# Kernel tuning notes

Hardware: AMD Instinct MI355X
Metric: run time of the kernel (lower is better)

The kernel has to match this reference:

```python
import jax, jax.numpy as jnp
import numpy as np

B, E, N, M = 2, 512, 4096, 4096

def setup_inputs() -> dict:
    key = jax.random.key(0)
    ks = jax.random.split(key, 8)
    s = 1.0 / np.sqrt(E)
    return {
        "src_embedding": jax.random.normal(ks[0], (B, E, N), jnp.float32),
        "tgt_embedding": jax.random.normal(ks[1], (B, E, M), jnp.float32),
        "src": jax.random.normal(ks[2], (B, 3, N), jnp.float32),
        "tgt": jax.random.normal(ks[3], (B, 3, M), jnp.float32),
        "Wq": jax.random.normal(ks[4], (E, E), jnp.float32) * s,
        "bq": jax.random.normal(ks[5], (E,), jnp.float32) * s,
        "Wk": jax.random.normal(ks[6], (E, E), jnp.float32) * s,
        "bk": jax.random.normal(ks[7], (E,), jnp.float32) * s,
    }

def reference(src_embedding, tgt_embedding, src, tgt, Wq, bq, Wk, bk):
    # query/key: [B, N, E] after transpose + Linear (y = x @ W^T + b)
    q = jnp.einsum('ben,fe->bnf', src_embedding, Wq) + bq
    k = jnp.einsum('bem,fe->bmf', tgt_embedding, Wk) + bk
    # pairwise_distance[b,n,m] = -||q_n||^2 + 2 q_n.k_m - ||k_m||^2 = -||q_n - k_m||^2
    inner = jnp.einsum('bne,bme->bnm', q, k)          # [B, N, M]
    qq = jnp.sum(q * q, axis=-1)                      # [B, N]
    kk = jnp.sum(k * k, axis=-1)                      # [B, M]
    pairwise = 2.0 * inner - qq[:, :, None] - kk[:, None, :]
    scores = jax.nn.softmax(pairwise, axis=2)         # softmax over keys (M)
    # src_corr = tgt @ scores^T : [B, 3, N]
    src_corr = jnp.einsum('bdm,bnm->bdn', tgt, scores)
    return (src, src_corr)
```

## Files before the change

### kernel.cpp

```cpp
#include <hip/hip_runtime.h>


typedef _Float16 f16;
typedef __attribute__((ext_vector_type(8))) _Float16 f16x8;
typedef __attribute__((ext_vector_type(4))) float f32x4;

constexpr int B_ = 2, E_ = 512, N_ = 4096, M_ = 4096;
constexpr int MCH = 8;
constexpr float WSCALE = 64.0f;

__device__ __forceinline__ f32x4 mfma16(f16x8 a, f16x8 b, f32x4 c) {
  return __builtin_amdgcn_mfma_f32_16x16x32_f16(a, b, c, 0, 0, 0);
}
__device__ __forceinline__ void gll16(const void* g, void* l) {
  __builtin_amdgcn_global_load_lds(
      (const __attribute__((address_space(1))) unsigned int*)g,
      (__attribute__((address_space(3))) unsigned int*)l, 16, 0, 0);
}
__device__ __forceinline__ void waitv8() { asm volatile("s_waitcnt vmcnt(8)" ::: "memory"); }
__device__ __forceinline__ void waitv0() { asm volatile("s_waitcnt vmcnt(0)" ::: "memory"); }
__device__ __forceinline__ f32x4 vmax4(f32x4 a, f32x4 b) {
  f32x4 r;
  r[0] = fmaxf(a[0], b[0]); r[1] = fmaxf(a[1], b[1]);
  r[2] = fmaxf(a[2], b[2]); r[3] = fmaxf(a[3], b[3]);
  return r;
}
__device__ __forceinline__ f32x4 vexp4(f32x4 a) {
  f32x4 r;
  r[0] = __expf(a[0]); r[1] = __expf(a[1]);
  r[2] = __expf(a[2]); r[3] = __expf(a[3]);
  return r;
}


__global__ void k_split_w(const float* __restrict__ Wq, const float* __restrict__ Wk,
                          f16* __restrict__ WqH, f16* __restrict__ WqL,
                          f16* __restrict__ WkH, f16* __restrict__ WkL) {
  int i = blockIdx.x * 256 + threadIdx.x;
  float a = Wq[i] * WSCALE;
  f16 ah = (f16)a; WqH[i] = ah; WqL[i] = (f16)(a - (float)ah);
  float b = Wk[i] * WSCALE;
  f16 bh = (f16)b; WkH[i] = bh; WkL[i] = (f16)(b - (float)bh);
}

__global__ void k_tsplit(const float* __restrict__ Xq, const float* __restrict__ Xk,
                         f16* __restrict__ XqH, f16* __restrict__ XqL,
                         f16* __restrict__ XkH, f16* __restrict__ XkL) {
  __shared__ float tile[64][65];
  const int b = blockIdx.z >> 1, which = blockIdx.z & 1;
  const float* X = (which ? Xk : Xq) + (size_t)b * E_ * N_;
  f16* H = (which ? XkH : XqH) + (size_t)b * N_ * E_;
  f16* L = (which ? XkL : XqL) + (size_t)b * N_ * E_;
  const int e0 = blockIdx.x * 64, n0 = blockIdx.y * 64;
  const int x = threadIdx.x, y = threadIdx.y;
#pragma unroll
  for (int j = 0; j < 16; ++j) {
    int e = y * 16 + j;
    tile[e][x] = X[(size_t)(e0 + e) * N_ + n0 + x];
  }
  __syncthreads();
#pragma unroll
  for (int j = 0; j < 16; ++j) {
    int nl = y * 16 + j;
    float v = tile[x][nl];
    f16 h = (f16)v;
    H[(size_t)(n0 + nl) * E_ + e0 + x] = h;
    L[(size_t)(n0 + nl) * E_ + e0 + x] = (f16)(v - (float)h);
  }
}

__global__ __launch_bounds__(256, 2) void k_proj(
    const f16* __restrict__ XqH, const f16* __restrict__ XqL,
    const f16* __restrict__ XkH, const f16* __restrict__ XkL,
    const f16* __restrict__ WqH, const f16* __restrict__ WqL,
    const f16* __restrict__ WkH, const f16* __restrict__ WkL,
    const float* __restrict__ bq, const float* __restrict__ bk,
    f16* __restrict__ QH, f16* __restrict__ QL,
    f16* __restrict__ KH, f16* __restrict__ KL,
    float* __restrict__ kkout) {
  __shared__ char lds[65536];
  const int b = blockIdx.z >> 1, kind = blockIdx.z & 1;
  const f16* AH = (kind ? XkH : XqH) + (size_t)b * N_ * E_;
  const f16* AL = (kind ? XkL : XqL) + (size_t)b * N_ * E_;
  const f16* BH = kind ? WkH : WqH;
  const f16* BL = kind ? WkL : WqL;
  const float* bias = kind ? bk : bq;
  f16* OH = (kind ? KH : QH) + (size_t)b * N_ * E_;
  f16* OL = (kind ? KL : QL) + (size_t)b * N_ * E_;
  const int n0 = blockIdx.x * 128, f0 = blockIdx.y * 128;
  const int l = threadIdx.x & 63, w = threadIdx.x >> 6;
  const int wr = (w >> 1) * 64, wc = (w & 1) * 64;
  const int r15 = l & 15;

  const int q = (l & 7) ^ (l >> 3);
  const size_t soff = (size_t)(w * 8 + (l >> 3)) * E_ + (q & 3) * 8;
  const f16* sA = (q < 4 ? AH : AL) + (size_t)n0 * E_ + soff;
  const f16* sB = (q < 4 ? BH : BL) + (size_t)f0 * E_ + soff;

  auto STAGE = [&](int k) {
    char* dA = lds + ((k & 1) << 14) + w * 1024;
    char* dB = lds + 32768 + ((k & 1) << 14) + w * 1024;
    const f16* pa = sA + k * 32;
    const f16* pb = sB + k * 32;
#pragma unroll
    for (int c = 0; c < 4; ++c) {
      gll16(pa + (size_t)c * 32 * E_, dA + c * 4096);
      gll16(pb + (size_t)c * 32 * E_, dB + c * 4096);
    }
  };

  const int pH16 = ((l >> 4) ^ (l & 7)) * 16;
  const int aoffH = (wr + r15) * 128 + pH16;
  const int boffH = (wc + r15) * 128 + pH16;

  f32x4 acc[4][4] = {};
  STAGE(0);
#pragma unroll 2
  for (int k = 0; k < 16; ++k) {
    if (k < 15) { STAGE(k + 1); waitv8(); } else { waitv0(); }
    __builtin_amdgcn_sched_barrier(0);
    __builtin_amdgcn_s_barrier();
    const char* cA = lds + ((k & 1) << 14);
    const char* cB = lds + 32768 + ((k & 1) << 14);
    f16x8 ah[4], al[4], bh[4], bl[4];
#pragma unroll
    for (int i = 0; i < 4; ++i) {
      ah[i] = *(const f16x8*)(cA + aoffH + i * 2048);
      al[i] = *(const f16x8*)(cA + (aoffH ^ 64) + i * 2048);
      bh[i] = *(const f16x8*)(cB + boffH + i * 2048);
      bl[i] = *(const f16x8*)(cB + (boffH ^ 64) + i * 2048);
    }
    __builtin_amdgcn_s_setprio(1);
#pragma unroll
    for (int i = 0; i < 4; ++i)
#pragma unroll
      for (int j = 0; j < 4; ++j) {
        acc[i][j] = mfma16(ah[i], bh[j], acc[i][j]);
        acc[i][j] = mfma16(ah[i], bl[j], acc[i][j]);
        acc[i][j] = mfma16(al[i], bh[j], acc[i][j]);
      }
    __builtin_amdgcn_s_setprio(0);
    __builtin_amdgcn_s_barrier();
  }

  const int rowg = (l >> 4) * 4;
  float kkp[4][4];
#pragma unroll
  for (int i = 0; i < 4; ++i)
#pragma unroll
    for (int r = 0; r < 4; ++r) kkp[i][r] = 0.f;
#pragma unroll
  for (int j = 0; j < 4; ++j) {
    int f = f0 + wc + j * 16 + r15;
    float bv = bias[f];
#pragma unroll
    for (int i = 0; i < 4; ++i) {
#pragma unroll
      for (int r = 0; r < 4; ++r) {
        int n = n0 + wr + i * 16 + rowg + r;
        float qv = acc[i][j][r] * (1.0f / WSCALE) + bv;
        f16 h = (f16)qv;
        OH[(size_t)n * E_ + f] = h;
        OL[(size_t)n * E_ + f] = (f16)(qv - (float)h);
        kkp[i][r] += qv * qv;
      }
    }
  }
  if (kind) {
#pragma unroll
    for (int i = 0; i < 4; ++i)
#pragma unroll
      for (int r = 0; r < 4; ++r) {
        float v = kkp[i][r];
        v += __shfl_xor(v, 1); v += __shfl_xor(v, 2);
        v += __shfl_xor(v, 4); v += __shfl_xor(v, 8);
        if (r15 == 0) {
          int n = n0 + wr + i * 16 + rowg + r;
          atomicAdd(&kkout[(size_t)b * M_ + n], v);
        }
      }
  }
}

__global__ __launch_bounds__(256, 2) void k_flash(
    const f16* __restrict__ QH, const f16* __restrict__ QL,
    const f16* __restrict__ KH, const f16* __restrict__ KL,
    const float* __restrict__ kk, const float* __restrict__ tgt,
    float* __restrict__ part) {
  __shared__ char lds[73728];
  float* ksw = (float*)(lds + 65536);
  const int b = blockIdx.z;
  const int n0 = blockIdx.x * 128;
  const int mc = blockIdx.y, m0c = mc * 512;
  const int tid = threadIdx.x, l = tid & 63, w = tid >> 6;
  const int r15 = l & 15;

  for (int idx = tid; idx < 512; idx += 256) {
    int mt = idx >> 7, rem = idx & 127, j = rem >> 4, rr = rem & 15;
    int dst = (mt * 16 + rr) * 8 + j;
    ksw[dst]        = kk[(size_t)b * M_ + m0c + idx];
    ksw[512 + dst]  = tgt[((size_t)b * 3 + 0) * M_ + m0c + idx];
    ksw[1024 + dst] = tgt[((size_t)b * 3 + 1) * M_ + m0c + idx];
    ksw[1536 + dst] = tgt[((size_t)b * 3 + 2) * M_ + m0c + idx];
  }
  __syncthreads();

  const f16* AH = QH + ((size_t)b * N_ + n0) * E_;
  const f16* AL = QL + ((size_t)b * N_ + n0) * E_;
  const f16* BHb = KH + ((size_t)b * M_ + m0c) * E_;
  const f16* BLb = KL + ((size_t)b * M_ + m0c) * E_;

  const int q = (l & 7) ^ (l >> 3);
  const size_t soff = (size_t)(w * 8 + (l >> 3)) * E_ + (q & 3) * 8;
  const f16* sA = (q < 4 ? AH : AL) + soff;
  const f16* sB = (q < 4 ? BHb : BLb) + soff;

  auto STAGE = [&](int s) {
    int mt_ = s >> 4, k_ = s & 15;
    char* dA = lds + ((s & 1) << 14) + w * 1024;
    char* dB = lds + 32768 + ((s & 1) << 14) + w * 1024;
    const f16* pa = sA + k_ * 32;
    const f16* pb = sB + (size_t)mt_ * 128 * E_ + k_ * 32;
#pragma unroll
    for (int c = 0; c < 4; ++c) {
      gll16(pa + (size_t)c * 32 * E_, dA + c * 4096);
      gll16(pb + (size_t)c * 32 * E_, dB + c * 4096);
    }
  };

  const int pH16 = ((l >> 4) ^ (l & 7)) * 16;
  const int aoffH = (w * 32 + r15) * 128 + pH16;
  const int boffH = r15 * 128 + pH16;

  f32x4 mrunA = {-3.0e38f, -3.0e38f, -3.0e38f, -3.0e38f};
  f32x4 mrunB = {-3.0e38f, -3.0e38f, -3.0e38f, -3.0e38f};
  f32x4 psumA = {}, p0A = {}, p1A = {}, p2A = {};
  f32x4 psumB = {}, p0B = {}, p1B = {}, p2B = {};

  auto BURST = [&](const f32x4 (&aP)[2][8], int i01, int pmt,
                   f32x4& mrun, f32x4& psum, f32x4& p0, f32x4& p1, f32x4& p2)
      __attribute__((always_inline)) {
    const float* bp = ksw + (pmt * 16 + r15) * 8;
    f32x4 kvL = *(const f32x4*)(bp);
    f32x4 kvH = *(const f32x4*)(bp + 4);
    f32x4 t0L = *(const f32x4*)(bp + 512),  t0H = *(const f32x4*)(bp + 516);
    f32x4 t1L = *(const f32x4*)(bp + 1024), t1H = *(const f32x4*)(bp + 1028);
    f32x4 t2L = *(const f32x4*)(bp + 1536), t2H = *(const f32x4*)(bp + 1540);
    float kv[8]  = {kvL[0], kvL[1], kvL[2], kvL[3], kvH[0], kvH[1], kvH[2], kvH[3]};
    float tv0[8] = {t0L[0], t0L[1], t0L[2], t0L[3], t0H[0], t0H[1], t0H[2], t0H[3]};
    float tv1[8] = {t1L[0], t1L[1], t1L[2], t1L[3], t1H[0], t1H[1], t1H[2], t1H[3]};
    float tv2[8] = {t2L[0], t2L[1], t2L[2], t2L[3], t2H[0], t2H[1], t2H[2], t2H[3]};
    f32x4 sv[8];
    f32x4 mx = {-3.0e38f, -3.0e38f, -3.0e38f, -3.0e38f};
#pragma unroll
    for (int j = 0; j < 8; ++j) {
      sv[j] = 2.0f * aP[i01][j] - kv[j];
      mx = vmax4(mx, sv[j]);
    }
#pragma unroll
    for (int e = 0; e < 4; ++e) {
      float v = mx[e];
      v = fmaxf(v, __shfl_xor(v, 1)); v = fmaxf(v, __shfl_xor(v, 2));
      v = fmaxf(v, __shfl_xor(v, 4)); v = fmaxf(v, __shfl_xor(v, 8));
      mx[e] = v;
    }
    f32x4 nm = vmax4(mrun, mx);
    f32x4 sc = vexp4(mrun - nm);
    mrun = nm;
    psum *= sc; p0 *= sc; p1 *= sc; p2 *= sc;
#pragma unroll
    for (int j = 0; j < 8; ++j) {
      f32x4 e4 = vexp4(sv[j] - nm);
      psum += e4;
      p0 += e4 * tv0[j];
      p1 += e4 * tv1[j];
      p2 += e4 * tv2[j];
    }
  };

  auto TILE = [&](int mt, f32x4 (&acc)[2][8], const f32x4 (&aP)[2][8], bool doSM)
      __attribute__((always_inline)) {
#pragma unroll
    for (int i = 0; i < 2; ++i)
#pragma unroll
      for (int j = 0; j < 8; ++j) acc[i][j] = f32x4{0.f, 0.f, 0.f, 0.f};
#pragma unroll 2
    for (int k = 0; k < 16; ++k) {
      const int s = mt * 16 + k;
      if (s < 63) { STAGE(s + 1); waitv8(); } else { waitv0(); }
      __builtin_amdgcn_sched_barrier(0);
      __builtin_amdgcn_s_barrier();
      const char* cA = lds + ((s & 1) << 14);
      const char* cB = lds + 32768 + ((s & 1) << 14);
      f16x8 ah0 = *(const f16x8*)(cA + aoffH);
      f16x8 ah1 = *(const f16x8*)(cA + aoffH + 2048);
      f16x8 al0 = *(const f16x8*)(cA + (aoffH ^ 64));
      f16x8 al1 = *(const f16x8*)(cA + (aoffH ^ 64) + 2048);
      __builtin_amdgcn_s_setprio(1);
#pragma unroll
      for (int j = 0; j < 8; ++j) {
        f16x8 bh = *(const f16x8*)(cB + boffH + j * 2048);
        f16x8 bl = *(const f16x8*)(cB + (boffH ^ 64) + j * 2048);
        acc[0][j] = mfma16(ah0, bh, acc[0][j]);
        acc[1][j] = mfma16(ah1, bh, acc[1][j]);
        acc[0][j] = mfma16(ah0, bl, acc[0][j]);
        acc[1][j] = mfma16(ah1, bl, acc[1][j]);
        acc[0][j] = mfma16(al0, bh, acc[0][j]);
        acc[1][j] = mfma16(al1, bh, acc[1][j]);
      }
      __builtin_amdgcn_s_setprio(0);
      __builtin_amdgcn_s_barrier();
      if (doSM && k == 7)  BURST(aP, 0, mt - 1, mrunA, psumA, p0A, p1A, p2A);
      if (doSM && k == 15) BURST(aP, 1, mt - 1, mrunB, psumB, p0B, p1B, p2B);
    }
  };

  f32x4 accE[2][8], accO[2][8];
  STAGE(0);
  TILE(0, accE, accO, false);
  TILE(1, accO, accE, true);
  TILE(2, accE, accO, true);
  TILE(3, accO, accE, true);
  BURST(accO, 0, 3, mrunA, psumA, p0A, p1A, p2A);
  BURST(accO, 1, 3, mrunB, psumB, p0B, p1B, p2B);

  auto RED = [&](f32x4& v) __attribute__((always_inline)) {
#pragma unroll
    for (int e = 0; e < 4; ++e) {
      float x = v[e];
      x += __shfl_xor(x, 1); x += __shfl_xor(x, 2);
      x += __shfl_xor(x, 4); x += __shfl_xor(x, 8);
      v[e] = x;
    }
  };
  RED(psumA); RED(p0A); RED(p1A); RED(p2A);
  RED(psumB); RED(p0B); RED(p1B); RED(p2B);

  if (r15 == 0) {
    const int hi = l >> 4;
#pragma unroll
    for (int i = 0; i < 2; ++i)
#pragma unroll
      for (int r = 0; r < 4; ++r) {
        int n = n0 + w * 32 + i * 16 + hi * 4 + r;
        size_t pb = ((size_t)(b * N_ + n) * MCH + mc) * 5;
        part[pb + 0] = i ? mrunB[r] : mrunA[r];
        part[pb + 1] = i ? psumB[r] : psumA[r];
        part[pb + 2] = i ? p0B[r] : p0A[r];
        part[pb + 3] = i ? p1B[r] : p1A[r];
        part[pb + 4] = i ? p2B[r] : p2A[r];
      }
  }
}

__global__ void k_out(const float* __restrict__ part, const float* __restrict__ src,
                      float* __restrict__ out) {
  int gid = blockIdx.x * 256 + threadIdx.x;
  if (blockIdx.x < B_ * N_ / 256) {
    int idx = gid;
    int b = idx >> 12, n = idx & (N_ - 1);
    const float* p = part + (size_t)idx * MCH * 5;
    float M = -3.0e38f;
#pragma unroll
    for (int c = 0; c < MCH; ++c) M = fmaxf(M, p[c * 5]);
    float S = 0.f, P0 = 0.f, P1 = 0.f, P2 = 0.f;
#pragma unroll
    for (int c = 0; c < MCH; ++c) {
      float e = __expf(p[c * 5] - M);
      S += p[c * 5 + 1] * e;
      P0 += p[c * 5 + 2] * e;
      P1 += p[c * 5 + 3] * e;
      P2 += p[c * 5 + 4] * e;
    }
    float inv = 1.0f / S;
    float* oc = out + (size_t)B_ * 3 * N_;
    oc[((size_t)b * 3 + 0) * N_ + n] = P0 * inv;
    oc[((size_t)b * 3 + 1) * N_ + n] = P1 * inv;
    oc[((size_t)b * 3 + 2) * N_ + n] = P2 * inv;
  } else {
    int i = gid - B_ * N_;
    out[i] = src[i];
  }
}

extern "C" void kernel_launch(void* const* d_in, const int* in_sizes, int n_in,
                              void* d_out, int out_size, void* d_ws, size_t ws_size,
                              hipStream_t stream) {
  const float* src_emb = (const float*)d_in[0];
  const float* tgt_emb = (const float*)d_in[1];
  const float* src     = (const float*)d_in[2];
  const float* tgt     = (const float*)d_in[3];
  const float* Wq      = (const float*)d_in[4];
  const float* bq      = (const float*)d_in[5];
  const float* Wk      = (const float*)d_in[6];
  const float* bk      = (const float*)d_in[7];
  float* out = (float*)d_out;

  constexpr size_t SZX = (size_t)B_ * N_ * E_;
  constexpr size_t OFFW = 4 * SZX * sizeof(f16);
  constexpr size_t OFFQ = OFFW + 4 * (size_t)E_ * E_ * sizeof(f16);
  constexpr size_t OFFK2 = OFFQ + 4 * SZX * sizeof(f16);
  constexpr size_t OFFP = OFFK2 + (size_t)B_ * M_ * sizeof(float);
  constexpr size_t NEED = OFFP + (size_t)B_ * N_ * MCH * 5 * sizeof(float);
  if (ws_size < NEED) return;

  char* ws = (char*)d_ws;
  f16* XqH = (f16*)(ws);
  f16* XqL = XqH + SZX;
  f16* XkH = XqL + SZX;
  f16* XkL = XkH + SZX;
  f16* WqH = (f16*)(ws + OFFW);
  f16* WqL = WqH + (size_t)E_ * E_;
  f16* WkH = WqL + (size_t)E_ * E_;
  f16* WkL = WkH + (size_t)E_ * E_;
  f16* QH = (f16*)(ws + OFFQ);
  f16* QL = QH + SZX;
  f16* KH = QL + SZX;
  f16* KL = KH + SZX;
  float* kk = (float*)(ws + OFFK2);
  float* part = (float*)(ws + OFFP);

  k_split_w<<<dim3(E_ * E_ / 256), 256, 0, stream>>>(Wq, Wk, WqH, WqL, WkH, WkL);
  k_tsplit<<<dim3(E_ / 64, N_ / 64, B_ * 2), dim3(64, 4), 0, stream>>>(
      src_emb, tgt_emb, XqH, XqL, XkH, XkL);
  hipMemsetAsync(kk, 0, (size_t)B_ * M_ * sizeof(float), stream);
  k_proj<<<dim3(N_ / 128, E_ / 128, B_ * 2), 256, 0, stream>>>(
      XqH, XqL, XkH, XkL, WqH, WqL, WkH, WkL, bq, bk, QH, QL, KH, KL, kk);
  k_flash<<<dim3(N_ / 128, MCH, B_), 256, 0, stream>>>(QH, QL, KH, KL, kk, tgt, part);
  k_out<<<dim3(B_ * N_ / 256 + B_ * 3 * N_ / 256), 256, 0, stream>>>(part, src, out);
}
```

Before: 238.2 us.

## Keep Q fragments in registers, use 8 waves and triple-buffer K tiles

The flash kernel now runs 512 threads (8 waves), each wave owning 16 query rows. Its Q hi/lo fragments for the full E dimension are loaded once into registers instead of being streamed through LDS every step. Only K tiles are staged, through a 3-deep ring with a wait depth of two stages ahead. The softmax update runs once per 128-key tile instead of being interleaved as split bursts. This frees LDS and cuts redundant Q traffic, but it raises register pressure (32 f16x8 per thread under launch bounds 512,2) and gives up the previous overlap of softmax with MFMA work.

```diff
diff --git a/kernel.cpp b/kernel.cpp
--- a/kernel.cpp
+++ b/kernel.cpp
@@ -18,6 +18,8 @@
       (__attribute__((address_space(3))) unsigned int*)l, 16, 0, 0);
 }
 __device__ __forceinline__ void waitv8() { asm volatile("s_waitcnt vmcnt(8)" ::: "memory"); }
+__device__ __forceinline__ void waitv4() { asm volatile("s_waitcnt vmcnt(4)" ::: "memory"); }
+__device__ __forceinline__ void waitv2() { asm volatile("s_waitcnt vmcnt(2)" ::: "memory"); }
 __device__ __forceinline__ void waitv0() { asm volatile("s_waitcnt vmcnt(0)" ::: "memory"); }
 __device__ __forceinline__ f32x4 vmax4(f32x4 a, f32x4 b) {
   f32x4 r;
@@ -182,20 +184,21 @@
   }
 }
 
-__global__ __launch_bounds__(256, 2) void k_flash(
+__global__ __launch_bounds__(512, 2) void k_flash(
     const f16* __restrict__ QH, const f16* __restrict__ QL,
     const f16* __restrict__ KH, const f16* __restrict__ KL,
     const float* __restrict__ kk, const float* __restrict__ tgt,
     float* __restrict__ part) {
-  __shared__ char lds[73728];
-  float* ksw = (float*)(lds + 65536);
+  __shared__ char lds[57344];
+  float* ksw = (float*)(lds + 49152);
   const int b = blockIdx.z;
   const int n0 = blockIdx.x * 128;
   const int mc = blockIdx.y, m0c = mc * 512;
   const int tid = threadIdx.x, l = tid & 63, w = tid >> 6;
-  const int r15 = l & 15;
-
-  for (int idx = tid; idx < 512; idx += 256) {
+  const int r15 = l & 15, hi = l >> 4;
+
+  {
+    int idx = tid;
     int mt = idx >> 7, rem = idx & 127, j = rem >> 4, rr = rem & 15;
     int dst = (mt * 16 + rr) * 8 + j;
     ksw[dst]        = kk[(size_t)b * M_ + m0c + idx];
@@ -205,124 +208,97 @@
   }
   __syncthreads();
 
-  const f16* AH = QH + ((size_t)b * N_ + n0) * E_;
-  const f16* AL = QL + ((size_t)b * N_ + n0) * E_;
-  const f16* BHb = KH + ((size_t)b * M_ + m0c) * E_;
-  const f16* BLb = KL + ((size_t)b * M_ + m0c) * E_;
-
-  const int q = (l & 7) ^ (l >> 3);
-  const size_t soff = (size_t)(w * 8 + (l >> 3)) * E_ + (q & 3) * 8;
-  const f16* sA = (q < 4 ? AH : AL) + soff;
-  const f16* sB = (q < 4 ? BHb : BLb) + soff;
+  const size_t arow = ((size_t)b * N_ + n0 + w * 16 + r15) * E_ + hi * 8;
+  const f16* Agh = QH + arow;
+  const f16* Agl = QL + arow;
+  f16x8 ah[16], al[16];
+#pragma unroll
+  for (int k = 0; k < 16; ++k) {
+    ah[k] = *(const f16x8*)(Agh + k * 32);
+    al[k] = *(const f16x8*)(Agl + k * 32);
+  }
+
+  const int qq = (tid & 7) ^ ((tid >> 3) & 7);
+  const f16* KHb = KH + ((size_t)b * M_ + m0c) * E_;
+  const f16* KLb = KL + ((size_t)b * M_ + m0c) * E_;
+  const f16* sBr = (qq < 4 ? KHb : KLb) + (size_t)(tid >> 3) * E_ + (qq & 3) * 8;
 
   auto STAGE = [&](int s) {
-    int mt_ = s >> 4, k_ = s & 15;
-    char* dA = lds + ((s & 1) << 14) + w * 1024;
-    char* dB = lds + 32768 + ((s & 1) << 14) + w * 1024;
-    const f16* pa = sA + k_ * 32;
-    const f16* pb = sB + (size_t)mt_ * 128 * E_ + k_ * 32;
-#pragma unroll
-    for (int c = 0; c < 4; ++c) {
-      gll16(pa + (size_t)c * 32 * E_, dA + c * 4096);
-      gll16(pb + (size_t)c * 32 * E_, dB + c * 4096);
-    }
+    char* d = lds + (s % 3) * 16384 + tid * 16;
+    const f16* p = sBr + (size_t)((s >> 4) * 128) * E_ + (s & 15) * 32;
+    gll16(p, d);
+    gll16(p + (size_t)64 * E_, d + 8192);
   };
 
-  const int pH16 = ((l >> 4) ^ (l & 7)) * 16;
-  const int aoffH = (w * 32 + r15) * 128 + pH16;
-  const int boffH = r15 * 128 + pH16;
-
-  f32x4 mrunA = {-3.0e38f, -3.0e38f, -3.0e38f, -3.0e38f};
-  f32x4 mrunB = {-3.0e38f, -3.0e38f, -3.0e38f, -3.0e38f};
-  f32x4 psumA = {}, p0A = {}, p1A = {}, p2A = {};
-  f32x4 psumB = {}, p0B = {}, p1B = {}, p2B = {};
-
-  auto BURST = [&](const f32x4 (&aP)[2][8], int i01, int pmt,
-                   f32x4& mrun, f32x4& psum, f32x4& p0, f32x4& p1, f32x4& p2)
-      __attribute__((always_inline)) {
-    const float* bp = ksw + (pmt * 16 + r15) * 8;
-    f32x4 kvL = *(const f32x4*)(bp);
-    f32x4 kvH = *(const f32x4*)(bp + 4);
-    f32x4 t0L = *(const f32x4*)(bp + 512),  t0H = *(const f32x4*)(bp + 516);
-    f32x4 t1L = *(const f32x4*)(bp + 1024), t1H = *(const f32x4*)(bp + 1028);
-    f32x4 t2L = *(const f32x4*)(bp + 1536), t2H = *(const f32x4*)(bp + 1540);
-    float kv[8]  = {kvL[0], kvL[1], kvL[2], kvL[3], kvH[0], kvH[1], kvH[2], kvH[3]};
-    float tv0[8] = {t0L[0], t0L[1], t0L[2], t0L[3], t0H[0], t0H[1], t0H[2], t0H[3]};
-    float tv1[8] = {t1L[0], t1L[1], t1L[2], t1L[3], t1H[0], t1H[1], t1H[2], t1H[3]};
-    float tv2[8] = {t2L[0], t2L[1], t2L[2], t2L[3], t2H[0], t2H[1], t2H[2], t2H[3]};
-    f32x4 sv[8];
-    f32x4 mx = {-3.0e38f, -3.0e38f, -3.0e38f, -3.0e38f};
-#pragma unroll
-    for (int j = 0; j < 8; ++j) {
-      sv[j] = 2.0f * aP[i01][j] - kv[j];
-      mx = vmax4(mx, sv[j]);
-    }
-#pragma unroll
-    for (int e = 0; e < 4; ++e) {
-      float v = mx[e];
-      v = fmaxf(v, __shfl_xor(v, 1)); v = fmaxf(v, __shfl_xor(v, 2));
-      v = fmaxf(v, __shfl_xor(v, 4)); v = fmaxf(v, __shfl_xor(v, 8));
-      mx[e] = v;
-    }
-    f32x4 nm = vmax4(mrun, mx);
-    f32x4 sc = vexp4(mrun - nm);
-    mrun = nm;
-    psum *= sc; p0 *= sc; p1 *= sc; p2 *= sc;
-#pragma unroll
-    for (int j = 0; j < 8; ++j) {
-      f32x4 e4 = vexp4(sv[j] - nm);
-      psum += e4;
-      p0 += e4 * tv0[j];
-      p1 += e4 * tv1[j];
-      p2 += e4 * tv2[j];
-    }
-  };
-
-  auto TILE = [&](int mt, f32x4 (&acc)[2][8], const f32x4 (&aP)[2][8], bool doSM)
-      __attribute__((always_inline)) {
-#pragma unroll
-    for (int i = 0; i < 2; ++i)
-#pragma unroll
-      for (int j = 0; j < 8; ++j) acc[i][j] = f32x4{0.f, 0.f, 0.f, 0.f};
-#pragma unroll 2
+  const int boffH = r15 * 128 + ((hi ^ (l & 7)) * 16);
+
+  f32x4 acc[8];
+  f32x4 mrun = {-3.0e38f, -3.0e38f, -3.0e38f, -3.0e38f};
+  f32x4 psum = {}, p0 = {}, p1 = {}, p2 = {};
+
+  STAGE(0);
+  STAGE(1);
+
+#pragma unroll
+  for (int mt = 0; mt < 4; ++mt) {
+#pragma unroll
+    for (int j = 0; j < 8; ++j) acc[j] = f32x4{0.f, 0.f, 0.f, 0.f};
+#pragma unroll
     for (int k = 0; k < 16; ++k) {
       const int s = mt * 16 + k;
-      if (s < 63) { STAGE(s + 1); waitv8(); } else { waitv0(); }
+      if (s < 62) { STAGE(s + 2); waitv4(); }
+      else if (s == 62) waitv2();
+      else waitv0();
       __builtin_amdgcn_sched_barrier(0);
       __builtin_amdgcn_s_barrier();
-      const char* cA = lds + ((s & 1) << 14);
-      const char* cB = lds + 32768 + ((s & 1) << 14);
-      f16x8 ah0 = *(const f16x8*)(cA + aoffH);
-      f16x8 ah1 = *(const f16x8*)(cA + aoffH + 2048);
-      f16x8 al0 = *(const f16x8*)(cA + (aoffH ^ 64));
-      f16x8 al1 = *(const f16x8*)(cA + (aoffH ^ 64) + 2048);
+      const char* cB = lds + (s % 3) * 16384;
       __builtin_amdgcn_s_setprio(1);
 #pragma unroll
       for (int j = 0; j < 8; ++j) {
         f16x8 bh = *(const f16x8*)(cB + boffH + j * 2048);
         f16x8 bl = *(const f16x8*)(cB + (boffH ^ 64) + j * 2048);
-        acc[0][j] = mfma16(ah0, bh, acc[0][j]);
-        acc[1][j] = mfma16(ah1, bh, acc[1][j]);
-        acc[0][j] = mfma16(ah0, bl, acc[0][j]);
-        acc[1][j] = mfma16(ah1, bl, acc[1][j]);
-        acc[0][j] = mfma16(al0, bh, acc[0][j]);
-        acc[1][j] = mfma16(al1, bh, acc[1][j]);
+        acc[j] = mfma16(ah[k], bh, acc[j]);
+        acc[j] = mfma16(ah[k], bl, acc[j]);
+        acc[j] = mfma16(al[k], bh, acc[j]);
       }
       __builtin_amdgcn_s_setprio(0);
       __builtin_amdgcn_s_barrier();
-      if (doSM && k == 7)  BURST(aP, 0, mt - 1, mrunA, psumA, p0A, p1A, p2A);
-      if (doSM && k == 15) BURST(aP, 1, mt - 1, mrunB, psumB, p0B, p1B, p2B);
-    }
-  };
-
-  f32x4 accE[2][8], accO[2][8];
-  STAGE(0);
-  TILE(0, accE, accO, false);
-  TILE(1, accO, accE, true);
-  TILE(2, accE, accO, true);
-  TILE(3, accO, accE, true);
-  BURST(accO, 0, 3, mrunA, psumA, p0A, p1A, p2A);
-  BURST(accO, 1, 3, mrunB, psumB, p0B, p1B, p2B);
+    }
+
+    {
+      const float* bp = ksw + (mt * 16 + r15) * 8;
+      float kv[8], tv0[8], tv1[8], tv2[8];
+#pragma unroll
+      for (int j = 0; j < 8; ++j) {
+        kv[j] = bp[j];
+        tv0[j] = bp[512 + j];
+        tv1[j] = bp[1024 + j];
+        tv2[j] = bp[1536 + j];
+      }
+      f32x4 mx = {-3.0e38f, -3.0e38f, -3.0e38f, -3.0e38f};
+#pragma unroll
+      for (int j = 0; j < 8; ++j) mx = vmax4(mx, 2.0f * acc[j] - kv[j]);
+#pragma unroll
+      for (int e = 0; e < 4; ++e) {
+        float v = mx[e];
+        v = fmaxf(v, __shfl_xor(v, 1)); v = fmaxf(v, __shfl_xor(v, 2));
+        v = fmaxf(v, __shfl_xor(v, 4)); v = fmaxf(v, __shfl_xor(v, 8));
+        mx[e] = v;
+      }
+      f32x4 nm = vmax4(mrun, mx);
+      f32x4 sc = vexp4(mrun - nm);
+      mrun = nm;
+      psum *= sc; p0 *= sc; p1 *= sc; p2 *= sc;
+#pragma unroll
+      for (int j = 0; j < 8; ++j) {
+        f32x4 e4 = vexp4(2.0f * acc[j] - kv[j] - nm);
+        psum += e4;
+        p0 += e4 * tv0[j];
+        p1 += e4 * tv1[j];
+        p2 += e4 * tv2[j];
+      }
+    }
+  }
 
   auto RED = [&](f32x4& v) __attribute__((always_inline)) {
 #pragma unroll
@@ -333,23 +309,19 @@
       v[e] = x;
     }
   };
-  RED(psumA); RED(p0A); RED(p1A); RED(p2A);
-  RED(psumB); RED(p0B); RED(p1B); RED(p2B);
+  RED(psum); RED(p0); RED(p1); RED(p2);
 
   if (r15 == 0) {
-    const int hi = l >> 4;
-#pragma unroll
-    for (int i = 0; i < 2; ++i)
-#pragma unroll
-      for (int r = 0; r < 4; ++r) {
-        int n = n0 + w * 32 + i * 16 + hi * 4 + r;
-        size_t pb = ((size_t)(b * N_ + n) * MCH + mc) * 5;
-        part[pb + 0] = i ? mrunB[r] : mrunA[r];
-        part[pb + 1] = i ? psumB[r] : psumA[r];
-        part[pb + 2] = i ? p0B[r] : p0A[r];
-        part[pb + 3] = i ? p1B[r] : p1A[r];
-        part[pb + 4] = i ? p2B[r] : p2A[r];
-      }
+#pragma unroll
+    for (int r = 0; r < 4; ++r) {
+      int n = n0 + w * 16 + hi * 4 + r;
+      size_t pb = ((size_t)(b * N_ + n) * MCH + mc) * 5;
+      part[pb + 0] = mrun[r];
+      part[pb + 1] = psum[r];
+      part[pb + 2] = p0[r];
+      part[pb + 3] = p1[r];
+      part[pb + 4] = p2[r];
+    }
   }
 }
 
@@ -426,6 +398,6 @@
   hipMemsetAsync(kk, 0, (size_t)B_ * M_ * sizeof(float), stream);
   k_proj<<<dim3(N_ / 128, E_ / 128, B_ * 2), 256, 0, stream>>>(
       XqH, XqL, XkH, XkL, WqH, WqL, WkH, WkL, bq, bk, QH, QL, KH, KL, kk);
-  k_flash<<<dim3(N_ / 128, MCH, B_), 256, 0, stream>>>(QH, QL, KH, KL, kk, tgt, part);
+  k_flash<<<dim3(N_ / 128, MCH, B_), 512, 0, stream>>>(QH, QL, KH, KL, kk, tgt, part);
   k_out<<<dim3(B_ * N_ / 256 + B_ * 3 * N_ / 256), 256, 0, stream>>>(part, src, out);
 }
```

Result: no change. 237.0 us (-0.5%).
